# Optimization experiments

Hardware: AMD Instinct MI355X
Metric: run time of the kernel (lower is better)

## Reference

```python
import jax, jax.numpy as jnp
import numpy as np

N = 50000      # nodes
E = 1200000    # edges
G = 256        # graphs in batch
H = 64         # hidden_dim
F_IN = 5       # input_dim
L = 3          # num deep GCN layers
EPS_BN = 1e-5
EPS_MSG = 1e-7

def setup_inputs() -> dict:
    key = jax.random.key(0)
    ks = jax.random.split(key, 12)
    r = lambda i, shp, s=0.1: jax.random.normal(ks[i], shp, jnp.float32) * s
    return {
        "x": jax.random.normal(ks[0], (N, F_IN), jnp.float32),
        "edge_index": jax.random.randint(ks[1], (2, E), 0, N),
        "batch_idx": jnp.sort(jax.random.randint(ks[2], (N,), 0, G)),
        "conv1_W": r(3, (F_IN, H)), "conv1_b": jnp.zeros((H,), jnp.float32),
        "bn1_g": jnp.ones((H,), jnp.float32), "bn1_b": jnp.zeros((H,), jnp.float32),
        "ln_g": jnp.ones((L, H), jnp.float32), "ln_b": jnp.zeros((L, H), jnp.float32),
        "prelu_a": jnp.full((L, H), 0.25, jnp.float32),
        "gen_t": jnp.ones((L,), jnp.float32),
        "mlp_W1": r(4, (L, H, 2 * H)), "mlp_b1": jnp.zeros((L, 2 * H), jnp.float32),
        "mlp_bn_g": jnp.ones((L, 2 * H), jnp.float32), "mlp_bn_b": jnp.zeros((L, 2 * H), jnp.float32),
        "mlp_W2": r(5, (L, 2 * H, H)), "mlp_b2": jnp.zeros((L, H), jnp.float32),
        "lin1_W": r(6, ((L + 1) * H * 2, 2 * H)), "lin1_b": jnp.zeros((2 * H,), jnp.float32),
        "lin2_W": r(7, (2 * H, H)), "lin2_b": jnp.zeros((H,), jnp.float32),
        "out_W": r(8, (H, 1)), "out_b": jnp.zeros((1,), jnp.float32),
    }

def _layernorm(x, g, b):
    mu = jnp.mean(x, axis=-1, keepdims=True)
    var = jnp.mean(jnp.square(x - mu), axis=-1, keepdims=True)
    return (x - mu) * jax.lax.rsqrt(var + EPS_BN) * g + b

def _prelu(x, a):
    return jnp.where(x >= 0, x, a * x)

def _bn_eval(x, g, b):
    # eval-mode BatchNorm with running_mean=0, running_var=1
    return x * (g / jnp.sqrt(1.0 + EPS_BN)) + b

def reference(x, edge_index, batch_idx, conv1_W, conv1_b, bn1_g, bn1_b,
              ln_g, ln_b, prelu_a, gen_t, mlp_W1, mlp_b1, mlp_bn_g, mlp_bn_b,
              mlp_W2, mlp_b2, lin1_W, lin1_b, lin2_W, lin2_b, out_W, out_b):
    n = x.shape[0]
    src, dst = edge_index[0], edge_index[1]

    # ---- GCNConv (with self loops, symmetric normalization) ----
    loops = jnp.arange(n)
    row = jnp.concatenate([src, loops])  # [E+N]
    col = jnp.concatenate([dst, loops])
    h = x @ conv1_W
    deg = jax.ops.segment_sum(jnp.ones_like(col, jnp.float32), col, num_segments=n)
    dinv = jnp.where(deg > 0, deg ** -0.5, 0.0)
    norm = dinv[row] * dinv[col]
    h = jax.ops.segment_sum(h[row] * norm[:, None], col, num_segments=n) + conv1_b
    h = _bn_eval(h, bn1_g, bn1_b)
    h = jax.nn.relu(h)

    xs = [h]
    # ---- DeepGCNLayer (res+) x L, GENConv with softmax aggregation ----
    for i in range(ln_g.shape[0]):
        u = _layernorm(h, ln_g[i], ln_b[i])
        u = _prelu(u, prelu_a[i])
        msg = jax.nn.relu(u[src]) + EPS_MSG            # [E, H]
        sc = msg * gen_t[i]
        m = jax.ops.segment_max(sc, dst, num_segments=n)
        e = jnp.exp(sc - m[dst])
        s = jax.ops.segment_sum(e, dst, num_segments=n)
        alpha = e / s[dst]                             # segment-wise softmax per channel
        agg = jax.ops.segment_sum(msg * alpha, dst, num_segments=n) + u  # root add
        z = agg @ mlp_W1[i] + mlp_b1[i]
        z = _bn_eval(z, mlp_bn_g[i], mlp_bn_b[i])
        z = jax.nn.relu(z)
        z = z @ mlp_W2[i] + mlp_b2[i]
        h = h + z                                      # res+
        xs.append(h)

    # ---- JumpingKnowledge cat + global mean/max pool ----
    xc = jnp.concatenate(xs, axis=1)                   # [N, 4H]
    cnt = jax.ops.segment_sum(jnp.ones((n,), jnp.float32), batch_idx, num_segments=G)
    xmean = jax.ops.segment_sum(xc, batch_idx, num_segments=G) / jnp.maximum(cnt, 1.0)[:, None]
    xmax = jax.ops.segment_max(xc, batch_idx, num_segments=G)
    xmax = jnp.where(jnp.isfinite(xmax), xmax, 0.0)
    p = jnp.concatenate([xmean, xmax], axis=1)         # [G, 8H]

    # ---- readout MLP (dropout off in eval) ----
    p = jax.nn.relu(p @ lin1_W + lin1_b)
    p = jax.nn.relu(p @ lin2_W + lin2_b)
    return p @ out_W + out_b
```

## Files before the change

kernel.cpp:

```cpp
#include <hip/hip_runtime.h>
#include <math.h>

#define NND 50000
#define NE  1200000
#define NG  256
#define H   64
#define H2  128
#define H4  256
#define H8  512
#define FIN 5
#define EPS_BN 1e-5f
#define EPS_MSG 1e-7f
#define NB 196
#define TILES 196
#define TCAP 7168
#define EPB 4096
#define NB1 293
#define ELLC 72
#define PC 8
#define MT 64

typedef _Float16 half8 __attribute__((ext_vector_type(8)));
typedef _Float16 half4 __attribute__((ext_vector_type(4)));
typedef float floatx4 __attribute__((ext_vector_type(4)));


__global__ void k_setup(const int* __restrict__ batch, int* tilecur, int* __restrict__ gstart,
                        const float* __restrict__ x, float* __restrict__ xp,
                        const float* __restrict__ W1, const float* __restrict__ W2,
                        _Float16* __restrict__ w1f, _Float16* __restrict__ w2f) {
    int b = blockIdx.x, t = threadIdx.x;
    if (b < NB) {
        int n = b * 256 + t;
        if (n < NND) {
            float a0 = x[n * FIN + 0], a1 = x[n * FIN + 1], a2 = x[n * FIN + 2];
            float a3 = x[n * FIN + 3], a4 = x[n * FIN + 4];
            *(float4*)&xp[n * 8] = make_float4(a0, a1, a2, a3);
            *(float4*)&xp[n * 8 + 4] = make_float4(a4, 0.f, 0.f, 0.f);
        }
        return;
    }
    if (b == NB || b == NB + 1) {
        if (b == NB && t < TILES) tilecur[t] = 0;
        int g = (b - NB) * 256 + t;
        if (g > NG) return;
        int lo = 0, hi = NND;
        while (lo < hi) { int mid = (lo + hi) >> 1; if (batch[mid] < g) lo = mid + 1; else hi = mid; }
        gstart[g] = lo;
        return;
    }
    int tt = (b - NB - 2) * 256 + t;
    if (tt >= 3 * 16 * 64) return;
    int lane = tt & 63, fr = (tt >> 6) & 15, l = tt >> 10;
    {
        int jt = fr >> 1, kf = fr & 1;
        int j = jt * 16 + (lane & 15);
        int k0 = kf * 32 + (lane >> 4) * 8;
#pragma unroll
        for (int i = 0; i < 8; i++)
            w1f[(((size_t)l * 16 + jt * 2 + kf) * 64 + lane) * 8 + i] =
                (_Float16)W1[(size_t)l * H * H2 + (k0 + i) * H2 + j];
    }
    {
        int ct = fr >> 2, k2f = fr & 3;
        int c = ct * 16 + (lane & 15);
        int k0 = k2f * 32 + (lane >> 4) * 8;
#pragma unroll
        for (int i = 0; i < 8; i++)
            w2f[(((size_t)l * 16 + ct * 4 + k2f) * 64 + lane) * 8 + i] =
                (_Float16)W2[(size_t)l * H2 * H + (k0 + i) * H + c];
    }
}


__global__ void __launch_bounds__(256)
k_bin1(const int* __restrict__ ei, int* tilecur, unsigned* __restrict__ tilebuf) {
    __shared__ int cnt[TILES];
    __shared__ int base[TILES];
    int b = blockIdx.x, t = threadIdx.x;
    for (int i = t; i < TILES; i += 256) cnt[i] = 0;
    __syncthreads();
    int e0 = b * EPB;
#pragma unroll
    for (int r = 0; r < EPB / 256; r++) {
        int e = e0 + r * 256 + t;
        if (e < NE) atomicAdd(&cnt[ei[NE + e] >> 8], 1);
    }
    __syncthreads();
    for (int i = t; i < TILES; i += 256) {
        base[i] = atomicAdd(&tilecur[i], cnt[i]);
        cnt[i] = 0;
    }
    __syncthreads();
#pragma unroll
    for (int r = 0; r < EPB / 256; r++) {
        int e = e0 + r * 256 + t;
        if (e < NE) {
            int s = ei[e], d = ei[NE + e];
            int tile = d >> 8;
            int pos = base[tile] + atomicAdd(&cnt[tile], 1);
            if (pos < TCAP)
                tilebuf[(size_t)tile * TCAP + pos] = ((unsigned)s << 8) | (unsigned)(d & 255);
        }
    }
}

__global__ void __launch_bounds__(256)
k_bin2(const int* __restrict__ tilecur, const unsigned* __restrict__ tilebuf,
       unsigned short* __restrict__ ell, int* __restrict__ deg, float* __restrict__ dinv) {
    __shared__ unsigned short ell_l[256 * ELLC];
    __shared__ int cnt[256];
    int tile = blockIdx.x, t = threadIdx.x;
    cnt[t] = 0;
    __syncthreads();
    int n = min(tilecur[tile], TCAP);
    for (int i = t; i < n; i += 256) {
        unsigned v = tilebuf[(size_t)tile * TCAP + i];
        int dl = v & 255u;
        int slot = atomicAdd(&cnt[dl], 1);
        if (slot < ELLC) ell_l[dl * ELLC + slot] = (unsigned short)(v >> 8);
    }
    __syncthreads();
    const unsigned* s32 = (const unsigned*)ell_l;
    unsigned* d32 = (unsigned*)(ell + (size_t)tile * 256 * ELLC);
    for (int i = t; i < 256 * ELLC / 2; i += 256) d32[i] = s32[i];
    int d = tile * 256 + t;
    if (d < NND) {
        int c = min(cnt[t], ELLC);
        deg[d] = c;
        dinv[d] = rsqrtf((float)cnt[t] + 1.0f);
    }
}


__global__ void k_gcn(const int* __restrict__ deg, const unsigned short* __restrict__ ell,
                      const float* __restrict__ xp, const float* __restrict__ dinv,
                      const float* __restrict__ W,
                      const float* __restrict__ cb, const float* __restrict__ bg,
                      const float* __restrict__ bb,
                      const float* __restrict__ lg, const float* __restrict__ lb,
                      const float* __restrict__ pa,
                      float* __restrict__ xc, float* __restrict__ u,
                      _Float16* __restrict__ u_h) {
    int d = (blockIdx.x * blockDim.x + threadIdx.x) >> 6;
    int lane = threadIdx.x & 63;
    if (d >= NND) return;
    int dg = deg[d];
    size_t base = (size_t)d * ELLC;
    float xw0 = 0.f, xw1 = 0.f, xw2 = 0.f, xw3 = 0.f, xw4 = 0.f;
    for (int i = lane; i < dg; i += 64) {
        int s = (int)ell[base + i];
        float dv = dinv[s];
        float4 a = *(const float4*)&xp[s * 8];
        float a4 = xp[s * 8 + 4];
        xw0 += a.x * dv; xw1 += a.y * dv; xw2 += a.z * dv;
        xw3 += a.w * dv; xw4 += a4 * dv;
    }
#pragma unroll
    for (int off = 1; off <= 32; off <<= 1) {
        xw0 += __shfl_xor(xw0, off, 64);
        xw1 += __shfl_xor(xw1, off, 64);
        xw2 += __shfl_xor(xw2, off, 64);
        xw3 += __shfl_xor(xw3, off, 64);
        xw4 += __shfl_xor(xw4, off, 64);
    }
    float dd = dinv[d];
    float4 xa = *(const float4*)&xp[d * 8];
    float xa4 = xp[d * 8 + 4];
    xw0 += dd * xa.x; xw1 += dd * xa.y; xw2 += dd * xa.z;
    xw3 += dd * xa.w; xw4 += dd * xa4;
    float s_ = xw0 * W[0 * H + lane] + xw1 * W[1 * H + lane] + xw2 * W[2 * H + lane]
             + xw3 * W[3 * H + lane] + xw4 * W[4 * H + lane];
    float v = s_ * dd + cb[lane];
    v = v * (bg[lane] * rsqrtf(1.f + EPS_BN)) + bb[lane];
    float x0 = fmaxf(v, 0.f);
    xc[(size_t)d * H4 + lane] = x0;
    float sum = x0, sq = x0 * x0;
#pragma unroll
    for (int off = 32; off >= 1; off >>= 1) {
        sum += __shfl_xor(sum, off, 64);
        sq  += __shfl_xor(sq,  off, 64);
    }
    float mu  = sum * (1.f / H);
    float var = sq * (1.f / H) - mu * mu;
    float rs = rsqrtf(var + EPS_BN);
    float y = (x0 - mu) * rs * lg[lane] + lb[lane];
    y = (y >= 0.f) ? y : pa[lane] * y;
    u[d * H + lane] = y;
    u_h[(size_t)d * H + lane] = (_Float16)y;
}


__global__ void k_gen(const int* __restrict__ deg, const unsigned short* __restrict__ ell,
                      const float* __restrict__ u, const _Float16* __restrict__ u_h,
                      const float* __restrict__ tptr, int li, float* __restrict__ ua) {
    int d = (blockIdx.x * blockDim.x + threadIdx.x) >> 6;
    int lane = threadIdx.x & 63;
    if (d >= NND) return;
    int q = lane & 15, eg = lane >> 4;
    float t = tptr[li];
    int dg = deg[d];
    size_t base = (size_t)d * ELLC;
    float4 s4 = {0.f, 0.f, 0.f, 0.f}, n4 = {0.f, 0.f, 0.f, 0.f};
    for (int i0 = 0; i0 < dg; i0 += 64) {
        int idx = i0 + lane;
        int csrv = (idx < dg) ? (int)ell[base + idx] : 0;
        int chunk = min(64, dg - i0);
        for (int j = 0; j < chunk; j += 16) {
            half4 uv[4]; bool ok[4];
#pragma unroll
            for (int bb2 = 0; bb2 < 4; bb2++) {
                int e_rel = j + 4 * bb2 + eg;
                int s = __shfl(csrv, e_rel, 64);
                ok[bb2] = (e_rel < chunk);
                uv[bb2] = (half4){0, 0, 0, 0};
                if (ok[bb2]) uv[bb2] = *(const half4*)&u_h[(size_t)s * H + 4 * q];
            }
#pragma unroll
            for (int bb2 = 0; bb2 < 4; bb2++) {
                if (ok[bb2]) {
                    float m0 = fmaxf((float)uv[bb2][0], 0.f) + EPS_MSG;
                    float m1 = fmaxf((float)uv[bb2][1], 0.f) + EPS_MSG;
                    float m2 = fmaxf((float)uv[bb2][2], 0.f) + EPS_MSG;
                    float m3 = fmaxf((float)uv[bb2][3], 0.f) + EPS_MSG;
                    float e0 = __expf(m0 * t - 8.f);
                    float e1 = __expf(m1 * t - 8.f);
                    float e2 = __expf(m2 * t - 8.f);
                    float e3 = __expf(m3 * t - 8.f);
                    s4.x += e0; s4.y += e1; s4.z += e2; s4.w += e3;
                    n4.x += m0 * e0; n4.y += m1 * e1; n4.z += m2 * e2; n4.w += m3 * e3;
                }
            }
        }
    }
#pragma unroll
    for (int off = 16; off <= 32; off <<= 1) {
        s4.x += __shfl_xor(s4.x, off, 64); s4.y += __shfl_xor(s4.y, off, 64);
        s4.z += __shfl_xor(s4.z, off, 64); s4.w += __shfl_xor(s4.w, off, 64);
        n4.x += __shfl_xor(n4.x, off, 64); n4.y += __shfl_xor(n4.y, off, 64);
        n4.z += __shfl_xor(n4.z, off, 64); n4.w += __shfl_xor(n4.w, off, 64);
    }
    if (eg == 0) {
        float4 us = *(const float4*)&u[d * H + 4 * q];
        float4 o;
        o.x = us.x + ((s4.x > 0.f) ? n4.x / s4.x : 0.f);
        o.y = us.y + ((s4.y > 0.f) ? n4.y / s4.y : 0.f);
        o.z = us.z + ((s4.z > 0.f) ? n4.z / s4.z : 0.f);
        o.w = us.w + ((s4.w > 0.f) ? n4.w / s4.w : 0.f);
        *(float4*)&ua[d * H + 4 * q] = o;
    }
}


__global__ void __launch_bounds__(256)
k_mlp(const float* __restrict__ ua,
      const _Float16* __restrict__ w1f, const _Float16* __restrict__ w2f,
      const float* __restrict__ b1,
      const float* __restrict__ bng, const float* __restrict__ bnb,
      const float* __restrict__ b2,
      float* __restrict__ xc, int slice,
      const float* __restrict__ lg, const float* __restrict__ lb,
      const float* __restrict__ pa, float* __restrict__ u_next,
      _Float16* __restrict__ u_h, int do_ln) {
    __shared__ _Float16 a1[4][2][64][8];
    __shared__ _Float16 a2[4][4][64][8];
    int t = threadIdx.x;
    int w = t >> 6, l = t & 63;
    int nb = blockIdx.x * MT;
    int c_in = l & 15, quad = l >> 4;
    bool wvalid = (nb + 16 * w) < NND;

    {
        int n = t >> 2;
        int k0 = (t & 3) * 16;
        int gn = nb + n;
        float4 v0 = {0,0,0,0}, v1 = v0, v2 = v0, v3 = v0;
        if (gn < NND) {
            v0 = *(const float4*)&ua[gn * H + k0];
            v1 = *(const float4*)&ua[gn * H + k0 + 4];
            v2 = *(const float4*)&ua[gn * H + k0 + 8];
            v3 = *(const float4*)&ua[gn * H + k0 + 12];
        }
        int mt = n >> 4, kf = k0 >> 5, g0 = (k0 >> 3) & 3;
        half8 h0 = {(_Float16)v0.x, (_Float16)v0.y, (_Float16)v0.z, (_Float16)v0.w,
                    (_Float16)v1.x, (_Float16)v1.y, (_Float16)v1.z, (_Float16)v1.w};
        half8 h1 = {(_Float16)v2.x, (_Float16)v2.y, (_Float16)v2.z, (_Float16)v2.w,
                    (_Float16)v3.x, (_Float16)v3.y, (_Float16)v3.z, (_Float16)v3.w};
        *(half8*)&a1[mt][kf][(n & 15) + 16 * g0][0] = h0;
        *(half8*)&a1[mt][kf][(n & 15) + 16 * (g0 + 1)][0] = h1;
    }

    floatx4 acc[8];
#pragma unroll
    for (int jt = 0; jt < 8; jt++) acc[jt] = (floatx4){0.f, 0.f, 0.f, 0.f};
    half8 af0 = *(half8*)&a1[w][0][l][0];
    half8 af1 = *(half8*)&a1[w][1][l][0];
#pragma unroll
    for (int jt = 0; jt < 8; jt++) {
        half8 bf0 = *(const half8*)&w1f[((size_t)(jt * 2 + 0) * 64 + l) * 8];
        half8 bf1 = *(const half8*)&w1f[((size_t)(jt * 2 + 1) * 64 + l) * 8];
        acc[jt] = __builtin_amdgcn_mfma_f32_16x16x32_f16(af0, bf0, acc[jt], 0, 0, 0);
        acc[jt] = __builtin_amdgcn_mfma_f32_16x16x32_f16(af1, bf1, acc[jt], 0, 0, 0);
    }

    {
        float bns = rsqrtf(1.f + EPS_BN);
#pragma unroll
        for (int jt = 0; jt < 8; jt++) {
            int j = jt * 16 + c_in;
            float b1v = b1[j], bsv = bng[j] * bns, bbv = bnb[j];
            int kf2 = jt >> 1;
            int lp = 16 * ((2 * jt + (c_in >> 3)) & 3);
            int ii = c_in & 7;
#pragma unroll
            for (int reg = 0; reg < 4; reg++) {
                float z = fmaxf((acc[jt][reg] + b1v) * bsv + bbv, 0.f);
                a2[w][kf2][quad * 4 + reg + lp][ii] = (_Float16)z;
            }
        }
    }

    floatx4 acc2[4];
#pragma unroll
    for (int ct = 0; ct < 4; ct++) acc2[ct] = (floatx4){0.f, 0.f, 0.f, 0.f};
    half8 a2f[4];
#pragma unroll
    for (int k2f = 0; k2f < 4; k2f++) a2f[k2f] = *(half8*)&a2[w][k2f][l][0];
#pragma unroll
    for (int ct = 0; ct < 4; ct++) {
#pragma unroll
        for (int k2f = 0; k2f < 4; k2f++) {
            half8 bfr = *(const half8*)&w2f[((size_t)(ct * 4 + k2f) * 64 + l) * 8];
            acc2[ct] = __builtin_amdgcn_mfma_f32_16x16x32_f16(a2f[k2f], bfr, acc2[ct], 0, 0, 0);
        }
    }

    float vv[4][4];
#pragma unroll
    for (int ct = 0; ct < 4; ct++) {
        int c = ct * 16 + c_in;
        float b2v = b2[c];
#pragma unroll
        for (int reg = 0; reg < 4; reg++) {
            int node = nb + 16 * w + quad * 4 + reg;
            float v = 0.f;
            if (wvalid) {
                v = xc[(size_t)node * H4 + slice * H + c] + acc2[ct][reg] + b2v;
                xc[(size_t)node * H4 + (slice + 1) * H + c] = v;
            }
            vv[ct][reg] = v;
        }
    }
    if (do_ln) {
#pragma unroll
        for (int reg = 0; reg < 4; reg++) {
            float s = (vv[0][reg] + vv[1][reg]) + (vv[2][reg] + vv[3][reg]);
            float q = (vv[0][reg] * vv[0][reg] + vv[1][reg] * vv[1][reg]) +
                      (vv[2][reg] * vv[2][reg] + vv[3][reg] * vv[3][reg]);
#pragma unroll
            for (int off = 1; off <= 8; off <<= 1) {
                s += __shfl_xor(s, off, 64);
                q += __shfl_xor(q, off, 64);
            }
            float mu = s * (1.f / H);
            float var = q * (1.f / H) - mu * mu;
            float rs = rsqrtf(var + EPS_BN);
            int node = nb + 16 * w + quad * 4 + reg;
#pragma unroll
            for (int ct = 0; ct < 4; ct++) {
                int c = ct * 16 + c_in;
                float y = (vv[ct][reg] - mu) * rs * lg[c] + lb[c];
                y = (y >= 0.f) ? y : pa[c] * y;
                if (wvalid) {
                    u_next[node * H + c] = y;
                    u_h[(size_t)node * H + c] = (_Float16)y;
                }
            }
        }
    }
}


__global__ void __launch_bounds__(256)
k_pool1(const float* __restrict__ xc, const int* __restrict__ gstart,
        float* __restrict__ psum_p, float* __restrict__ pmax_p) {
    __shared__ float4 ssum[256];
    __shared__ float4 smax[256];
    int b = blockIdx.x;
    int g = b >> 3, k = b & (PC - 1);
    int t = threadIdx.x;
    int start = gstart[g], end = gstart[g + 1];
    int len = end - start;
    int c0 = start + (len * k) / PC;
    int c1 = start + (len * (k + 1)) / PC;
    int q = t & 63, sub = t >> 6;
    float4 sum = {0.f, 0.f, 0.f, 0.f};
    float4 mx = {-INFINITY, -INFINITY, -INFINITY, -INFINITY};
    for (int n = c0 + sub; n < c1; n += 4) {
        float4 v = *(const float4*)&xc[(size_t)n * H4 + 4 * q];
        sum.x += v.x; sum.y += v.y; sum.z += v.z; sum.w += v.w;
        mx.x = fmaxf(mx.x, v.x); mx.y = fmaxf(mx.y, v.y);
        mx.z = fmaxf(mx.z, v.z); mx.w = fmaxf(mx.w, v.w);
    }
    ssum[t] = sum; smax[t] = mx;
    __syncthreads();
    if (t < 64) {
        float4 s0 = ssum[t], s1 = ssum[t + 64], s2 = ssum[t + 128], s3 = ssum[t + 192];
        float4 m0 = smax[t], m1 = smax[t + 64], m2 = smax[t + 128], m3 = smax[t + 192];
        float4 S, M;
        S.x = (s0.x + s1.x) + (s2.x + s3.x);
        S.y = (s0.y + s1.y) + (s2.y + s3.y);
        S.z = (s0.z + s1.z) + (s2.z + s3.z);
        S.w = (s0.w + s1.w) + (s2.w + s3.w);
        M.x = fmaxf(fmaxf(m0.x, m1.x), fmaxf(m2.x, m3.x));
        M.y = fmaxf(fmaxf(m0.y, m1.y), fmaxf(m2.y, m3.y));
        M.z = fmaxf(fmaxf(m0.z, m1.z), fmaxf(m2.z, m3.z));
        M.w = fmaxf(fmaxf(m0.w, m1.w), fmaxf(m2.w, m3.w));
        *(float4*)&psum_p[(size_t)b * H4 + 4 * q] = S;
        *(float4*)&pmax_p[(size_t)b * H4 + 4 * q] = M;
    }
}

__global__ void __launch_bounds__(256)
k_readout(const float* __restrict__ psum_p, const float* __restrict__ pmax_p,
          const int* __restrict__ gstart,
          const float* __restrict__ W1, const float* __restrict__ b1,
          const float* __restrict__ W2, const float* __restrict__ b2,
          const float* __restrict__ Wo, const float* __restrict__ bo,
          float* __restrict__ out) {
    __shared__ float p0_l[H8];
    __shared__ float p1part[2][H2];
    __shared__ float p1_l[H2];
    __shared__ float p2part[4][H];
    __shared__ float p2_l[H];
    int g = blockIdx.x;
    int t = threadIdx.x;

    {
        float s = 0.f, m = -INFINITY;
#pragma unroll
        for (int k = 0; k < PC; k++) {
            s += psum_p[(size_t)(g * PC + k) * H4 + t];
            m = fmaxf(m, pmax_p[(size_t)(g * PC + k) * H4 + t]);
        }
        int cnt = gstart[g + 1] - gstart[g];
        p0_l[t] = s / fmaxf((float)cnt, 1.f);
        p0_l[H4 + t] = (cnt > 0) ? m : 0.f;
    }
    __syncthreads();

    {
        int j = t & 127, h = t >> 7;
        float acc = 0.f;
        int k0 = h * 256;
        for (int k = 0; k < 256; k++) acc += p0_l[k0 + k] * W1[(k0 + k) * H2 + j];
        p1part[h][j] = acc;
    }
    __syncthreads();
    if (t < H2) p1_l[t] = fmaxf(p1part[0][t] + p1part[1][t] + b1[t], 0.f);
    __syncthreads();

    {
        int c = t & 63, h = t >> 6;
        float acc = 0.f;
        int k0 = h * 32;
        for (int k = 0; k < 32; k++) acc += p1_l[k0 + k] * W2[(k0 + k) * H + c];
        p2part[h][c] = acc;
    }
    __syncthreads();
    if (t < H) p2_l[t] = fmaxf(((p2part[0][t] + p2part[1][t]) + (p2part[2][t] + p2part[3][t])) + b2[t], 0.f);
    __syncthreads();

    if (t < 64) {
        float v = p2_l[t] * Wo[t];
#pragma unroll
        for (int off = 32; off >= 1; off >>= 1) v += __shfl_xor(v, off, 64);
        if (t == 0) out[g] = v + bo[0];
    }
}

extern "C" void kernel_launch(void* const* d_in, const int* in_sizes, int n_in,
                              void* d_out, int out_size, void* d_ws, size_t ws_size,
                              hipStream_t stream) {
    const float* x       = (const float*)d_in[0];
    const int*   ei      = (const int*)d_in[1];
    const int*   batch   = (const int*)d_in[2];
    const float* conv1_W = (const float*)d_in[3];
    const float* conv1_b = (const float*)d_in[4];
    const float* bn1_g   = (const float*)d_in[5];
    const float* bn1_b   = (const float*)d_in[6];
    const float* ln_g    = (const float*)d_in[7];
    const float* ln_b    = (const float*)d_in[8];
    const float* prelu_a = (const float*)d_in[9];
    const float* gen_t   = (const float*)d_in[10];
    const float* mlp_W1  = (const float*)d_in[11];
    const float* mlp_b1  = (const float*)d_in[12];
    const float* mlp_bng = (const float*)d_in[13];
    const float* mlp_bnb = (const float*)d_in[14];
    const float* mlp_W2  = (const float*)d_in[15];
    const float* mlp_b2  = (const float*)d_in[16];
    const float* lin1_W  = (const float*)d_in[17];
    const float* lin1_b  = (const float*)d_in[18];
    const float* lin2_W  = (const float*)d_in[19];
    const float* lin2_b  = (const float*)d_in[20];
    const float* out_W   = (const float*)d_in[21];
    const float* out_b   = (const float*)d_in[22];
    float* out = (float*)d_out;

    float* ws   = (float*)d_ws;
    float* xc   = ws;
    float* u    = xc + (size_t)NND * H4;
    float* ua   = u + (size_t)NND * H;
    float* xp   = ua + (size_t)NND * H;
    float* dinv = xp + (size_t)NND * 8;
    int* deg    = (int*)(dinv + NND);
    int* gstart = deg + NND;
    int* tilecur = gstart + NG + 1;
    unsigned* tilebuf = (unsigned*)(tilecur + TILES);
    unsigned short* ell = (unsigned short*)(tilebuf + (size_t)TILES * TCAP);
    uintptr_t wb = (uintptr_t)(ell + (size_t)TILES * 256 * ELLC);
    wb = (wb + 15) & ~(uintptr_t)15;
    _Float16* w1f = (_Float16*)wb;
    _Float16* w2f = w1f + 3 * 8192;
    _Float16* u_h = w2f + 3 * 8192;
    uintptr_t pb = (uintptr_t)(u_h + (size_t)NND * H);
    pb = (pb + 15) & ~(uintptr_t)15;
    float* psum_p = (float*)pb;
    float* pmax_p = psum_p + (size_t)NG * PC * H4;

    const int B = 256;
    const int gNH  = (NND * H) / B;
    const int gMLP = (NND + MT - 1) / MT;

    k_setup<<<NB + 2 + 12, B, 0, stream>>>(batch, tilecur, gstart, x, xp,
                                           mlp_W1, mlp_W2, w1f, w2f);
    k_bin1<<<NB1, B, 0, stream>>>(ei, tilecur, tilebuf);
    k_bin2<<<TILES, B, 0, stream>>>(tilecur, tilebuf, ell, deg, dinv);

    k_gcn<<<gNH, B, 0, stream>>>(deg, ell, xp, dinv, conv1_W, conv1_b, bn1_g, bn1_b,
                                 ln_g, ln_b, prelu_a, xc, u, u_h);

    for (int i = 0; i < 3; i++) {
        k_gen<<<gNH, B, 0, stream>>>(deg, ell, u, u_h, gen_t, i, ua);
        int do_ln = (i < 2) ? 1 : 0;
        k_mlp<<<gMLP, B, 0, stream>>>(ua,
                                      w1f + (size_t)i * 8192, w2f + (size_t)i * 8192,
                                      mlp_b1 + i * H2,
                                      mlp_bng + i * H2, mlp_bnb + i * H2,
                                      mlp_b2 + i * H,
                                      xc, i,
                                      ln_g + (i + 1) * H, ln_b + (i + 1) * H,
                                      prelu_a + (i + 1) * H, u, u_h, do_ln);
    }

    k_pool1<<<NG * PC, B, 0, stream>>>(xc, gstart, psum_p, pmax_p);
    k_readout<<<NG, B, 0, stream>>>(psum_p, pmax_p, gstart,
                                    lin1_W, lin1_b, lin2_W, lin2_b, out_W, out_b, out);
}
```

Before: 347.6 us.

## Drop fp32 activation copies and pass fp16 between gen and mlp kernels

Removes the fp32 node-feature buffer u and the fp32 aggregate ua. The root term in k_gen is read from the fp16 copy, k_gen writes an fp16 aggregate, and k_mlp loads fp16 directly instead of converting fp32. This cuts global write and read traffic per layer. The gather loop in k_gen is also unrolled to 8 outstanding loads instead of 4. The cost is extra rounding on the residual/root-add path, which could affect accuracy.

```diff
diff --git a/kernel.cpp b/kernel.cpp
--- a/kernel.cpp
+++ b/kernel.cpp
@@ -126,8 +126,7 @@
     for (int i = t; i < 256 * ELLC / 2; i += 256) d32[i] = s32[i];
     int d = tile * 256 + t;
     if (d < NND) {
-        int c = min(cnt[t], ELLC);
-        deg[d] = c;
+        deg[d] = min(cnt[t], ELLC);
         dinv[d] = rsqrtf((float)cnt[t] + 1.0f);
     }
 }
@@ -140,8 +139,7 @@
                       const float* __restrict__ bb,
                       const float* __restrict__ lg, const float* __restrict__ lb,
                       const float* __restrict__ pa,
-                      float* __restrict__ xc, float* __restrict__ u,
-                      _Float16* __restrict__ u_h) {
+                      float* __restrict__ xc, _Float16* __restrict__ u_h) {
     int d = (blockIdx.x * blockDim.x + threadIdx.x) >> 6;
     int lane = threadIdx.x & 63;
     if (d >= NND) return;
@@ -186,14 +184,13 @@
     float rs = rsqrtf(var + EPS_BN);
     float y = (x0 - mu) * rs * lg[lane] + lb[lane];
     y = (y >= 0.f) ? y : pa[lane] * y;
-    u[d * H + lane] = y;
     u_h[(size_t)d * H + lane] = (_Float16)y;
 }
 
 
 __global__ void k_gen(const int* __restrict__ deg, const unsigned short* __restrict__ ell,
-                      const float* __restrict__ u, const _Float16* __restrict__ u_h,
-                      const float* __restrict__ tptr, int li, float* __restrict__ ua) {
+                      const _Float16* __restrict__ u_h,
+                      const float* __restrict__ tptr, int li, _Float16* __restrict__ ua_h) {
     int d = (blockIdx.x * blockDim.x + threadIdx.x) >> 6;
     int lane = threadIdx.x & 63;
     if (d >= NND) return;
@@ -206,23 +203,23 @@
         int idx = i0 + lane;
         int csrv = (idx < dg) ? (int)ell[base + idx] : 0;
         int chunk = min(64, dg - i0);
-        for (int j = 0; j < chunk; j += 16) {
-            half4 uv[4]; bool ok[4];
-#pragma unroll
-            for (int bb2 = 0; bb2 < 4; bb2++) {
-                int e_rel = j + 4 * bb2 + eg;
+        for (int j = 0; j < chunk; j += 32) {
+            half4 uv[8]; bool ok[8];
+#pragma unroll
+            for (int b2 = 0; b2 < 8; b2++) {
+                int e_rel = j + 4 * b2 + eg;
                 int s = __shfl(csrv, e_rel, 64);
-                ok[bb2] = (e_rel < chunk);
-                uv[bb2] = (half4){0, 0, 0, 0};
-                if (ok[bb2]) uv[bb2] = *(const half4*)&u_h[(size_t)s * H + 4 * q];
+                ok[b2] = (e_rel < chunk);
+                uv[b2] = (half4){0, 0, 0, 0};
+                if (ok[b2]) uv[b2] = *(const half4*)&u_h[(size_t)s * H + 4 * q];
             }
 #pragma unroll
-            for (int bb2 = 0; bb2 < 4; bb2++) {
-                if (ok[bb2]) {
-                    float m0 = fmaxf((float)uv[bb2][0], 0.f) + EPS_MSG;
-                    float m1 = fmaxf((float)uv[bb2][1], 0.f) + EPS_MSG;
-                    float m2 = fmaxf((float)uv[bb2][2], 0.f) + EPS_MSG;
-                    float m3 = fmaxf((float)uv[bb2][3], 0.f) + EPS_MSG;
+            for (int b2 = 0; b2 < 8; b2++) {
+                if (ok[b2]) {
+                    float m0 = fmaxf((float)uv[b2][0], 0.f) + EPS_MSG;
+                    float m1 = fmaxf((float)uv[b2][1], 0.f) + EPS_MSG;
+                    float m2 = fmaxf((float)uv[b2][2], 0.f) + EPS_MSG;
+                    float m3 = fmaxf((float)uv[b2][3], 0.f) + EPS_MSG;
                     float e0 = __expf(m0 * t - 8.f);
                     float e1 = __expf(m1 * t - 8.f);
                     float e2 = __expf(m2 * t - 8.f);
@@ -241,27 +238,26 @@
         n4.z += __shfl_xor(n4.z, off, 64); n4.w += __shfl_xor(n4.w, off, 64);
     }
     if (eg == 0) {
-        float4 us = *(const float4*)&u[d * H + 4 * q];
-        float4 o;
-        o.x = us.x + ((s4.x > 0.f) ? n4.x / s4.x : 0.f);
-        o.y = us.y + ((s4.y > 0.f) ? n4.y / s4.y : 0.f);
-        o.z = us.z + ((s4.z > 0.f) ? n4.z / s4.z : 0.f);
-        o.w = us.w + ((s4.w > 0.f) ? n4.w / s4.w : 0.f);
-        *(float4*)&ua[d * H + 4 * q] = o;
+        half4 us = *(const half4*)&u_h[(size_t)d * H + 4 * q];
+        float o0 = (float)us[0] + ((s4.x > 0.f) ? n4.x / s4.x : 0.f);
+        float o1 = (float)us[1] + ((s4.y > 0.f) ? n4.y / s4.y : 0.f);
+        float o2 = (float)us[2] + ((s4.z > 0.f) ? n4.z / s4.z : 0.f);
+        float o3 = (float)us[3] + ((s4.w > 0.f) ? n4.w / s4.w : 0.f);
+        half4 oh = {(_Float16)o0, (_Float16)o1, (_Float16)o2, (_Float16)o3};
+        *(half4*)&ua_h[(size_t)d * H + 4 * q] = oh;
     }
 }
 
 
 __global__ void __launch_bounds__(256)
-k_mlp(const float* __restrict__ ua,
+k_mlp(const _Float16* __restrict__ ua_h,
       const _Float16* __restrict__ w1f, const _Float16* __restrict__ w2f,
       const float* __restrict__ b1,
       const float* __restrict__ bng, const float* __restrict__ bnb,
       const float* __restrict__ b2,
       float* __restrict__ xc, int slice,
       const float* __restrict__ lg, const float* __restrict__ lb,
-      const float* __restrict__ pa, float* __restrict__ u_next,
-      _Float16* __restrict__ u_h, int do_ln) {
+      const float* __restrict__ pa, _Float16* __restrict__ u_h, int do_ln) {
     __shared__ _Float16 a1[4][2][64][8];
     __shared__ _Float16 a2[4][4][64][8];
     int t = threadIdx.x;
@@ -274,18 +270,12 @@
         int n = t >> 2;
         int k0 = (t & 3) * 16;
         int gn = nb + n;
-        float4 v0 = {0,0,0,0}, v1 = v0, v2 = v0, v3 = v0;
+        half8 h0 = {0,0,0,0,0,0,0,0}, h1 = h0;
         if (gn < NND) {
-            v0 = *(const float4*)&ua[gn * H + k0];
-            v1 = *(const float4*)&ua[gn * H + k0 + 4];
-            v2 = *(const float4*)&ua[gn * H + k0 + 8];
-            v3 = *(const float4*)&ua[gn * H + k0 + 12];
+            h0 = *(const half8*)&ua_h[(size_t)gn * H + k0];
+            h1 = *(const half8*)&ua_h[(size_t)gn * H + k0 + 8];
         }
         int mt = n >> 4, kf = k0 >> 5, g0 = (k0 >> 3) & 3;
-        half8 h0 = {(_Float16)v0.x, (_Float16)v0.y, (_Float16)v0.z, (_Float16)v0.w,
-                    (_Float16)v1.x, (_Float16)v1.y, (_Float16)v1.z, (_Float16)v1.w};
-        half8 h1 = {(_Float16)v2.x, (_Float16)v2.y, (_Float16)v2.z, (_Float16)v2.w,
-                    (_Float16)v3.x, (_Float16)v3.y, (_Float16)v3.z, (_Float16)v3.w};
         *(half8*)&a1[mt][kf][(n & 15) + 16 * g0][0] = h0;
         *(half8*)&a1[mt][kf][(n & 15) + 16 * (g0 + 1)][0] = h1;
     }
@@ -371,10 +361,7 @@
                 int c = ct * 16 + c_in;
                 float y = (vv[ct][reg] - mu) * rs * lg[c] + lb[c];
                 y = (y >= 0.f) ? y : pa[c] * y;
-                if (wvalid) {
-                    u_next[node * H + c] = y;
-                    u_h[(size_t)node * H + c] = (_Float16)y;
-                }
+                if (wvalid) u_h[(size_t)node * H + c] = (_Float16)y;
             }
         }
     }
@@ -509,9 +496,7 @@
 
     float* ws   = (float*)d_ws;
     float* xc   = ws;
-    float* u    = xc + (size_t)NND * H4;
-    float* ua   = u + (size_t)NND * H;
-    float* xp   = ua + (size_t)NND * H;
+    float* xp   = xc + (size_t)NND * H4;
     float* dinv = xp + (size_t)NND * 8;
     int* deg    = (int*)(dinv + NND);
     int* gstart = deg + NND;
@@ -522,8 +507,9 @@
     wb = (wb + 15) & ~(uintptr_t)15;
     _Float16* w1f = (_Float16*)wb;
     _Float16* w2f = w1f + 3 * 8192;
-    _Float16* u_h = w2f + 3 * 8192;
-    uintptr_t pb = (uintptr_t)(u_h + (size_t)NND * H);
+    _Float16* u_h  = w2f + 3 * 8192;
+    _Float16* ua_h = u_h + (size_t)NND * H;
+    uintptr_t pb = (uintptr_t)(ua_h + (size_t)NND * H);
     pb = (pb + 15) & ~(uintptr_t)15;
     float* psum_p = (float*)pb;
     float* pmax_p = psum_p + (size_t)NG * PC * H4;
@@ -538,19 +524,19 @@
     k_bin2<<<TILES, B, 0, stream>>>(tilecur, tilebuf, ell, deg, dinv);
 
     k_gcn<<<gNH, B, 0, stream>>>(deg, ell, xp, dinv, conv1_W, conv1_b, bn1_g, bn1_b,
-                                 ln_g, ln_b, prelu_a, xc, u, u_h);
+                                 ln_g, ln_b, prelu_a, xc, u_h);
 
     for (int i = 0; i < 3; i++) {
-        k_gen<<<gNH, B, 0, stream>>>(deg, ell, u, u_h, gen_t, i, ua);
+        k_gen<<<gNH, B, 0, stream>>>(deg, ell, u_h, gen_t, i, ua_h);
         int do_ln = (i < 2) ? 1 : 0;
-        k_mlp<<<gMLP, B, 0, stream>>>(ua,
+        k_mlp<<<gMLP, B, 0, stream>>>(ua_h,
                                       w1f + (size_t)i * 8192, w2f + (size_t)i * 8192,
                                       mlp_b1 + i * H2,
                                       mlp_bng + i * H2, mlp_bnb + i * H2,
                                       mlp_b2 + i * H,
                                       xc, i,
                                       ln_g + (i + 1) * H, ln_b + (i + 1) * H,
-                                      prelu_a + (i + 1) * H, u, u_h, do_ln);
+                                      prelu_a + (i + 1) * H, u_h, do_ln);
     }
 
     k_pool1<<<NG * PC, B, 0, stream>>>(xc, gstart, psum_p, pmax_p);
```

After: 339.6 us. 1.02x faster.
